# Kernel optimization log

Measured on AMD Instinct MI355X. Metric: run time of the kernel, lower is better.

Reference implementation:

```python
import jax, jax.numpy as jnp
import numpy as np

N = 100000
E = 1600000
IN_DIM = 128
EDGE_DIM = 32
H = 4
C = 32  # out_vertex_dim per head; concat output = H*C = 128


def setup_inputs() -> dict:
    key = jax.random.key(0)
    ks = jax.random.split(key, 12)
    point_attr = jax.random.normal(ks[0], (N, IN_DIM), dtype=jnp.float32)
    edge_index = jax.random.randint(ks[1], (2, E), 0, N, dtype=jnp.int64)
    edge_attr = jax.random.normal(ks[2], (E, EDGE_DIM), dtype=jnp.float32)
    # GATConv params (lin shared for src/dst when in_channels is int; bias separate)
    g = lambda k, shp, fan: jax.random.normal(k, shp, dtype=jnp.float32) * np.float32(1.0 / np.sqrt(fan))
    W = g(ks[3], (IN_DIM, H * C), IN_DIM)          # lin weight (no bias in PyG GATConv lin)
    att_src = g(ks[4], (H, C), C)
    att_dst = g(ks[5], (H, C), C)
    W_edge = g(ks[6], (EDGE_DIM, H * C), EDGE_DIM)  # lin_edge (bias=False)
    att_edge = g(ks[7], (H, C), C)
    bias = jnp.zeros((H * C,), dtype=jnp.float32)
    ln_gamma = jnp.ones((H * C,), dtype=jnp.float32)
    ln_beta = jnp.zeros((H * C,), dtype=jnp.float32)
    return {"point_attr": point_attr, "edge_index": edge_index, "edge_attr": edge_attr,
            "W": W, "att_src": att_src, "att_dst": att_dst, "W_edge": W_edge,
            "att_edge": att_edge, "bias": bias, "ln_gamma": ln_gamma, "ln_beta": ln_beta}


def reference(point_attr, edge_index, edge_attr, W, att_src, att_dst, W_edge, att_edge, bias, ln_gamma, ln_beta):
    n = point_attr.shape[0]
    x = (point_attr @ W).reshape(n, H, C)                      # [N,H,C]
    a_src = jnp.sum(x * att_src[None], axis=-1)                # [N,H]
    a_dst = jnp.sum(x * att_dst[None], axis=-1)                # [N,H]
    src, dst = edge_index[0], edge_index[1]
    e = (edge_attr @ W_edge).reshape(-1, H, C)                 # [E,H,C]
    a_edge = jnp.sum(e * att_edge[None], axis=-1)              # [E,H]
    alpha = a_src[src] + a_dst[dst] + a_edge                   # [E,H]
    alpha = jax.nn.leaky_relu(alpha, 0.2)                      # GATConv negative_slope
    amax = jax.ops.segment_max(alpha, dst, num_segments=n)
    expa = jnp.exp(alpha - amax[dst])
    asum = jax.ops.segment_sum(expa, dst, num_segments=n)
    attw = expa / (asum[dst] + 1e-16)                          # segment softmax over dst
    msg = x[src] * attw[:, :, None]                            # [E,H,C] gather+scale
    out = jax.ops.segment_sum(msg, dst, num_segments=n).reshape(n, H * C) + bias
    # LayerNorm(H*C)
    mu = jnp.mean(out, axis=-1, keepdims=True)
    var = jnp.mean((out - mu) ** 2, axis=-1, keepdims=True)
    out = (out - mu) / jnp.sqrt(var + 1e-5) * ln_gamma + ln_beta
    return jax.nn.leaky_relu(out, 0.01)                        # nn.LeakyReLU default slope
```

## Files before the change

kernel.cpp:

```cpp
#include <hip/hip_runtime.h>
#include <hip/hip_bf16.h>

#define IN_DIM 128
#define HC 128
#define NH 4
#define CH 32
#define EDGE_DIM 32
#define CAP 48

typedef short s8v __attribute__((ext_vector_type(8)));
typedef float f4v __attribute__((ext_vector_type(4)));

__device__ __forceinline__ unsigned pack_bf16(float a, float b) {
    unsigned ua = __float_as_uint(a), ub = __float_as_uint(b);
    ua += 0x7fffu + ((ua >> 16) & 1u);
    ub += 0x7fffu + ((ub >> 16) & 1u);
    return (ua >> 16) | (ub & 0xffff0000u);
}
__device__ __forceinline__ unsigned short bf16_1(float a) {
    unsigned ua = __float_as_uint(a);
    ua += 0x7fffu + ((ua >> 16) & 1u);
    return (unsigned short)(ua >> 16);
}

__global__ __launch_bounds__(256) void k_vp(
    const float* __restrict__ W_edge, const float* __restrict__ att_edge,
    float* __restrict__ v_edge, const float* __restrict__ W,
    unsigned short* __restrict__ Wt)
{
    int b = blockIdx.x, t = threadIdx.x;
    if (b == 64) {
        if (t < 128) {
            int h = t >> 5, k = t & 31;
            float s = 0.f;
            #pragma unroll
            for (int c = 0; c < CH; ++c)
                s += W_edge[k * HC + h * CH + c] * att_edge[h * CH + c];
            v_edge[h * EDGE_DIM + k] = s;
        }
    } else {
        int id = b * 256 + t;
        int n = id >> 7, k = id & 127;
        Wt[n * 128 + k] = bf16_1(W[k * 128 + n]);
    }
}

__global__ __launch_bounds__(256) void k_phase1(
    const float* __restrict__ edge_attr, const int* __restrict__ ei,
    const float* __restrict__ v_edge, int* __restrict__ cnt,
    int4* __restrict__ slots,
    const float* __restrict__ A, const unsigned short* __restrict__ Wt,
    unsigned short* __restrict__ xb16, int N, int E, int nbEdge)
{
    __shared__ unsigned Al[64 * 64];
    __shared__ float vl[HC];

    int t = threadIdx.x;

    if (blockIdx.x < nbEdge) {
        if (t < HC) vl[t] = v_edge[t];
        __syncthreads();
        int e = blockIdx.x * 256 + t;
        if (e >= E) return;
        const float4* ea4 = (const float4*)edge_attr + (size_t)e * 8;
        float ae[4] = {0.f, 0.f, 0.f, 0.f};
        #pragma unroll
        for (int j = 0; j < 8; ++j) {
            float4 v = ea4[j];
            #pragma unroll
            for (int h = 0; h < 4; ++h) {
                const float* vh = &vl[h * 32 + j * 4];
                ae[h] += v.x * vh[0] + v.y * vh[1] + v.z * vh[2] + v.w * vh[3];
            }
        }
        int src = ei[e], dst = ei[E + e];
        int pos = atomicAdd(&cnt[dst], 1);
        if (pos < CAP) {
            int4 pk;
            pk.x = src;
            pk.y = (int)pack_bf16(ae[0], ae[1]);
            pk.z = (int)pack_bf16(ae[2], ae[3]);
            pk.w = 0;
            slots[(size_t)dst * CAP + pos] = pk;
        }
    } else {
        int node0 = (blockIdx.x - nbEdge) * 64;
        const float4* A4 = (const float4*)A;
        #pragma unroll
        for (int it = 0; it < 8; ++it) {
            int id = it * 256 + t;
            int row = id >> 5, c = id & 31;
            float4 v = {0.f, 0.f, 0.f, 0.f};
            if (node0 + row < N) v = A4[(size_t)(node0 + row) * 32 + c];
            unsigned u0 = pack_bf16(v.x, v.y);
            unsigned u1 = pack_bf16(v.z, v.w);
            int k2 = 2 * c;
            int slot = k2 >> 2;
            int idx = ((slot ^ (row & 15)) << 2) | (k2 & 3);
            Al[row * 64 + idx]     = u0;
            Al[row * 64 + idx + 1] = u1;
        }
        __syncthreads();

        int l = t & 63;
        int w = t >> 6;
        int lrow = l & 15;
        int lk   = l >> 4;

        s8v afr[4];
        #pragma unroll
        for (int kb = 0; kb < 4; ++kb) {
            int slot = kb * 4 + lk;
            const unsigned* p = &Al[(w * 16 + lrow) * 64 + ((slot ^ lrow) << 2)];
            afr[kb] = *(const s8v*)p;
        }

        #pragma unroll
        for (int ct = 0; ct < 8; ++ct) {
            int col = ct * 16 + lrow;
            f4v acc = {0.f, 0.f, 0.f, 0.f};
            #pragma unroll
            for (int kb = 0; kb < 4; ++kb) {
                s8v bfr = *(const s8v*)&Wt[col * 128 + kb * 32 + lk * 8];
                acc = __builtin_amdgcn_mfma_f32_16x16x32_bf16(afr[kb], bfr, acc, 0, 0, 0);
            }
            #pragma unroll
            for (int r = 0; r < 4; ++r) {
                int node = node0 + w * 16 + lk * 4 + r;
                if (node < N) xb16[(size_t)node * 128 + col] = bf16_1(acc[r]);
            }
        }
    }
}

__global__ __launch_bounds__(256) void k_att(
    const unsigned* __restrict__ xb, const float* __restrict__ att_src,
    const float* __restrict__ att_dst, float* __restrict__ a_src,
    float* __restrict__ a_dst, int N)
{
    int t = threadIdx.x;
    int node = blockIdx.x * 16 + (t >> 4);
    int lane = t & 15;
    if (node >= N) return;
    const uint4* x4 = (const uint4*)xb;
    uint4 xv = x4[(size_t)node * 16 + lane];
    int c = lane * 8;
    float xs[8];
    xs[0] = __uint_as_float(xv.x << 16); xs[1] = __uint_as_float(xv.x & 0xffff0000u);
    xs[2] = __uint_as_float(xv.y << 16); xs[3] = __uint_as_float(xv.y & 0xffff0000u);
    xs[4] = __uint_as_float(xv.z << 16); xs[5] = __uint_as_float(xv.z & 0xffff0000u);
    xs[6] = __uint_as_float(xv.w << 16); xs[7] = __uint_as_float(xv.w & 0xffff0000u);
    float ps = 0.f, pd = 0.f;
    #pragma unroll
    for (int i = 0; i < 8; ++i) {
        ps += xs[i] * att_src[c + i];
        pd += xs[i] * att_dst[c + i];
    }
    ps += __shfl_xor(ps, 1); ps += __shfl_xor(ps, 2);
    pd += __shfl_xor(pd, 1); pd += __shfl_xor(pd, 2);
    if ((lane & 3) == 0) {
        a_src[node * 4 + (lane >> 2)] = ps;
        a_dst[node * 4 + (lane >> 2)] = pd;
    }
}

__global__ __launch_bounds__(256) void k_agg(
    const int* __restrict__ cnt, const int4* __restrict__ slots,
    const float* __restrict__ a_src, const float* __restrict__ a_dst,
    const unsigned* __restrict__ xb, const float* __restrict__ bias,
    const float* __restrict__ gamma, const float* __restrict__ beta,
    float* __restrict__ out, int N)
{
    int t = threadIdx.x;
    int node = blockIdx.x * 16 + (t >> 4);
    int lane = t & 15;
    if (node >= N) return;
    int st = node * CAP;
    int deg = cnt[node]; if (deg > CAP) deg = CAP;
    int en = st + deg;
    int hsel = lane >> 2;
    float adst = a_dst[node * 4 + hsel];
    const uint4* x4 = (const uint4*)xb;
    float acc[8] = {0.f, 0.f, 0.f, 0.f, 0.f, 0.f, 0.f, 0.f};
    float denom = 0.f;

    int s_c[4]; float ae_c[4], as_c[4];

    if (st < en) {
        #pragma unroll
        for (int j = 0; j < 4; ++j) {
            bool v = (st + j) < en;
            int a = v ? (st + j) : st;
            int4 pk = slots[a];
            s_c[j] = pk.x;
            unsigned w = (hsel & 2) ? (unsigned)pk.z : (unsigned)pk.y;
            float e = __uint_as_float((hsel & 1) ? (w & 0xffff0000u) : (w << 16));
            ae_c[j] = v ? e : -1e30f;
        }
        #pragma unroll
        for (int j = 0; j < 4; ++j) as_c[j] = a_src[s_c[j] * 4 + hsel];

        for (int p = st; p < en; p += 4) {
            int pn = p + 4;
            int s_n[4]; float ae_n[4], as_n[4];
            #pragma unroll
            for (int j = 0; j < 4; ++j) {
                bool v = (pn + j) < en;
                int a = v ? (pn + j) : st;
                int4 pk = slots[a];
                s_n[j] = pk.x;
                unsigned w = (hsel & 2) ? (unsigned)pk.z : (unsigned)pk.y;
                float e = __uint_as_float((hsel & 1) ? (w & 0xffff0000u) : (w << 16));
                ae_n[j] = v ? e : -1e30f;
            }
            #pragma unroll
            for (int j = 0; j < 4; ++j) as_n[j] = a_src[s_n[j] * 4 + hsel];

            #pragma unroll
            for (int j = 0; j < 4; ++j) {
                float al = as_c[j] + adst + ae_c[j];
                al = (al < 0.f) ? 0.2f * al : al;
                float ex = __expf(al);
                denom += ex;
                uint4 xv = x4[(size_t)s_c[j] * 16 + lane];
                acc[0] += ex * __uint_as_float(xv.x << 16);
                acc[1] += ex * __uint_as_float(xv.x & 0xffff0000u);
                acc[2] += ex * __uint_as_float(xv.y << 16);
                acc[3] += ex * __uint_as_float(xv.y & 0xffff0000u);
                acc[4] += ex * __uint_as_float(xv.z << 16);
                acc[5] += ex * __uint_as_float(xv.z & 0xffff0000u);
                acc[6] += ex * __uint_as_float(xv.w << 16);
                acc[7] += ex * __uint_as_float(xv.w & 0xffff0000u);
            }
            #pragma unroll
            for (int j = 0; j < 4; ++j) {
                s_c[j] = s_n[j]; ae_c[j] = ae_n[j]; as_c[j] = as_n[j];
            }
        }
    }
    float inv = 1.f / (denom + 1e-16f);
    int c = lane * 8;
    float4 b0 = *(const float4*)&bias[c];
    float4 b1 = *(const float4*)&bias[c + 4];
    float o[8];
    o[0] = acc[0] * inv + b0.x; o[1] = acc[1] * inv + b0.y;
    o[2] = acc[2] * inv + b0.z; o[3] = acc[3] * inv + b0.w;
    o[4] = acc[4] * inv + b1.x; o[5] = acc[5] * inv + b1.y;
    o[6] = acc[6] * inv + b1.z; o[7] = acc[7] * inv + b1.w;

    float s = 0.f;
    #pragma unroll
    for (int i = 0; i < 8; ++i) s += o[i];
    #pragma unroll
    for (int m = 1; m < 16; m <<= 1) s += __shfl_xor(s, m, 16);
    float mu = s * (1.0f / 128.0f);
    float q = 0.f;
    #pragma unroll
    for (int i = 0; i < 8; ++i) { o[i] -= mu; q += o[i] * o[i]; }
    #pragma unroll
    for (int m = 1; m < 16; m <<= 1) q += __shfl_xor(q, m, 16);
    float rstd = rsqrtf(q * (1.0f / 128.0f) + 1e-5f);
    float4 g0 = *(const float4*)&gamma[c];
    float4 g1 = *(const float4*)&gamma[c + 4];
    float4 e0 = *(const float4*)&beta[c];
    float4 e1 = *(const float4*)&beta[c + 4];
    float y[8];
    y[0] = o[0] * rstd * g0.x + e0.x; y[1] = o[1] * rstd * g0.y + e0.y;
    y[2] = o[2] * rstd * g0.z + e0.z; y[3] = o[3] * rstd * g0.w + e0.w;
    y[4] = o[4] * rstd * g1.x + e1.x; y[5] = o[5] * rstd * g1.y + e1.y;
    y[6] = o[6] * rstd * g1.z + e1.z; y[7] = o[7] * rstd * g1.w + e1.w;
    #pragma unroll
    for (int i = 0; i < 8; ++i) y[i] = (y[i] < 0.f) ? 0.01f * y[i] : y[i];
    float4 r0 = {y[0], y[1], y[2], y[3]};
    float4 r1 = {y[4], y[5], y[6], y[7]};
    float4* op = (float4*)out + (size_t)node * 32 + lane * 2;
    op[0] = r0;
    op[1] = r1;
}

extern "C" void kernel_launch(void* const* d_in, const int* in_sizes, int n_in,
                              void* d_out, int out_size, void* d_ws, size_t ws_size,
                              hipStream_t stream) {
    const float* point_attr = (const float*)d_in[0];
    const int*   edge_index = (const int*)d_in[1];
    const float* edge_attr  = (const float*)d_in[2];
    const float* W          = (const float*)d_in[3];
    const float* att_src    = (const float*)d_in[4];
    const float* att_dst    = (const float*)d_in[5];
    const float* W_edge     = (const float*)d_in[6];
    const float* att_edge   = (const float*)d_in[7];
    const float* bias       = (const float*)d_in[8];
    const float* ln_gamma   = (const float*)d_in[9];
    const float* ln_beta    = (const float*)d_in[10];

    int N = in_sizes[0] / IN_DIM;
    int E = in_sizes[2] / EDGE_DIM;
    float* out = (float*)d_out;

    char* ws = (char*)d_ws;
    size_t off = 0;
    auto alloc = [&](size_t bytes) {
        void* p = ws + off;
        off += (bytes + 255) & ~(size_t)255;
        return p;
    };
    unsigned* xb     = (unsigned*)alloc((size_t)N * 128 * 2);
    float* a_src     = (float*)alloc((size_t)N * 4 * 4);
    float* a_dst     = (float*)alloc((size_t)N * 4 * 4);
    int*   cnt       = (int*)alloc((size_t)N * 4);
    float* v_edge    = (float*)alloc(128 * 4);
    unsigned short* Wt = (unsigned short*)alloc(128 * 128 * 2);
    int4*  slots     = (int4*)alloc((size_t)N * CAP * 16);

    hipMemsetAsync(cnt, 0, (size_t)N * 4, stream);

    int nbEdge = (E + 255) / 256;
    int nbGemm = (N + 63) / 64;
    int nbAtt  = (N + 15) / 16;

    k_vp<<<65, 256, 0, stream>>>(W_edge, att_edge, v_edge, W, Wt);
    k_phase1<<<nbEdge + nbGemm, 256, 0, stream>>>(
        edge_attr, edge_index, v_edge, cnt, slots,
        point_attr, Wt, (unsigned short*)xb, N, E, nbEdge);
    k_att<<<nbAtt, 256, 0, stream>>>(xb, att_src, att_dst, a_src, a_dst, N);
    k_agg<<<nbAtt, 256, 0, stream>>>(cnt, slots, a_src, a_dst, xb,
                                     bias, ln_gamma, ln_beta, out, N);
}
```

Measured before the change: 247.6 us.

## Fuse attention-score dot products into GEMM epilogue and stage edge_attr through LDS

Removes the separate k_att kernel. a_src and a_dst are now computed from the fp32 MFMA accumulators in the projection GEMM's epilogue and reduced with cross-lane shuffles, which saves a launch and a full re-read of the bf16 x buffer. In the edge path, each block now loads its edge_attr tile with coalesced float4 reads into XOR-swizzled shared memory, replacing per-thread strided 128-byte row reads. In exchange, shared memory per block rises to about 33 KB and register pressure in the GEMM path goes up. The attention scores are also computed from unrounded fp32 values instead of bf16 x.

```diff
diff --git a/kernel.cpp b/kernel.cpp
--- a/kernel.cpp
+++ b/kernel.cpp
@@ -50,28 +50,46 @@
     const float* __restrict__ v_edge, int* __restrict__ cnt,
     int4* __restrict__ slots,
     const float* __restrict__ A, const unsigned short* __restrict__ Wt,
-    unsigned short* __restrict__ xb16, int N, int E, int nbEdge)
+    unsigned short* __restrict__ xb16,
+    const float* __restrict__ att_src, const float* __restrict__ att_dst,
+    float* __restrict__ a_src, float* __restrict__ a_dst,
+    int N, int E, int nbEdge)
 {
-    __shared__ unsigned Al[64 * 64];
-    __shared__ float vl[HC];
-
+    __shared__ __align__(16) char smem_[32768 + 512];
     int t = threadIdx.x;
 
     if (blockIdx.x < nbEdge) {
+        float* se = (float*)smem_;
+        float* vl = (float*)(smem_ + 32768);
+
+        const float4* eab4 = (const float4*)edge_attr + (size_t)blockIdx.x * 2048;
+        int rem = E - blockIdx.x * 256;
+        int nf4 = (rem >= 256) ? 2048 : ((rem > 0) ? rem * 8 : 0);
+        #pragma unroll
+        for (int it = 0; it < 8; ++it) {
+            int idx = it * 256 + t;
+            float4 f = {0.f, 0.f, 0.f, 0.f};
+            if (idx < nf4) f = eab4[idx];
+            int edge = idx >> 3, p4 = idx & 7, sw = edge & 31;
+            float* bp = &se[edge * 32];
+            bp[(p4 * 4 + 0) ^ sw] = f.x;
+            bp[(p4 * 4 + 1) ^ sw] = f.y;
+            bp[(p4 * 4 + 2) ^ sw] = f.z;
+            bp[(p4 * 4 + 3) ^ sw] = f.w;
+        }
         if (t < HC) vl[t] = v_edge[t];
         __syncthreads();
+
         int e = blockIdx.x * 256 + t;
         if (e >= E) return;
-        const float4* ea4 = (const float4*)edge_attr + (size_t)e * 8;
+        int sw = t & 31;
+        const float* bp = &se[t * 32];
         float ae[4] = {0.f, 0.f, 0.f, 0.f};
         #pragma unroll
-        for (int j = 0; j < 8; ++j) {
-            float4 v = ea4[j];
-            #pragma unroll
-            for (int h = 0; h < 4; ++h) {
-                const float* vh = &vl[h * 32 + j * 4];
-                ae[h] += v.x * vh[0] + v.y * vh[1] + v.z * vh[2] + v.w * vh[3];
-            }
+        for (int i = 0; i < 32; ++i) {
+            float x = bp[i ^ sw];
+            #pragma unroll
+            for (int h = 0; h < 4; ++h) ae[h] += x * vl[h * 32 + i];
         }
         int src = ei[e], dst = ei[E + e];
         int pos = atomicAdd(&cnt[dst], 1);
@@ -84,6 +102,7 @@
             slots[(size_t)dst * CAP + pos] = pk;
         }
     } else {
+        unsigned* Al = (unsigned*)smem_;
         int node0 = (blockIdx.x - nbEdge) * 64;
         const float4* A4 = (const float4*)A;
         #pragma unroll
@@ -115,6 +134,12 @@
             afr[kb] = *(const s8v*)p;
         }
 
+        float ps[4][4], pd[4][4];
+        #pragma unroll
+        for (int r = 0; r < 4; ++r)
+            #pragma unroll
+            for (int h = 0; h < 4; ++h) { ps[r][h] = 0.f; pd[r][h] = 0.f; }
+
         #pragma unroll
         for (int ct = 0; ct < 8; ++ct) {
             int col = ct * 16 + lrow;
@@ -124,43 +149,43 @@
                 s8v bfr = *(const s8v*)&Wt[col * 128 + kb * 32 + lk * 8];
                 acc = __builtin_amdgcn_mfma_f32_16x16x32_bf16(afr[kb], bfr, acc, 0, 0, 0);
             }
+            float av = att_src[col], dv = att_dst[col];
+            #pragma unroll
+            for (int r = 0; r < 4; ++r) {
+                ps[r][ct >> 1] += acc[r] * av;
+                pd[r][ct >> 1] += acc[r] * dv;
+            }
             #pragma unroll
             for (int r = 0; r < 4; ++r) {
                 int node = node0 + w * 16 + lk * 4 + r;
                 if (node < N) xb16[(size_t)node * 128 + col] = bf16_1(acc[r]);
             }
         }
-    }
-}
-
-__global__ __launch_bounds__(256) void k_att(
-    const unsigned* __restrict__ xb, const float* __restrict__ att_src,
-    const float* __restrict__ att_dst, float* __restrict__ a_src,
-    float* __restrict__ a_dst, int N)
-{
-    int t = threadIdx.x;
-    int node = blockIdx.x * 16 + (t >> 4);
-    int lane = t & 15;
-    if (node >= N) return;
-    const uint4* x4 = (const uint4*)xb;
-    uint4 xv = x4[(size_t)node * 16 + lane];
-    int c = lane * 8;
-    float xs[8];
-    xs[0] = __uint_as_float(xv.x << 16); xs[1] = __uint_as_float(xv.x & 0xffff0000u);
-    xs[2] = __uint_as_float(xv.y << 16); xs[3] = __uint_as_float(xv.y & 0xffff0000u);
-    xs[4] = __uint_as_float(xv.z << 16); xs[5] = __uint_as_float(xv.z & 0xffff0000u);
-    xs[6] = __uint_as_float(xv.w << 16); xs[7] = __uint_as_float(xv.w & 0xffff0000u);
-    float ps = 0.f, pd = 0.f;
-    #pragma unroll
-    for (int i = 0; i < 8; ++i) {
-        ps += xs[i] * att_src[c + i];
-        pd += xs[i] * att_dst[c + i];
-    }
-    ps += __shfl_xor(ps, 1); ps += __shfl_xor(ps, 2);
-    pd += __shfl_xor(pd, 1); pd += __shfl_xor(pd, 2);
-    if ((lane & 3) == 0) {
-        a_src[node * 4 + (lane >> 2)] = ps;
-        a_dst[node * 4 + (lane >> 2)] = pd;
+
+        #pragma unroll
+        for (int r = 0; r < 4; ++r)
+            #pragma unroll
+            for (int h = 0; h < 4; ++h) {
+                float vs = ps[r][h], vd = pd[r][h];
+                #pragma unroll
+                for (int m = 1; m <= 8; m <<= 1) {
+                    vs += __shfl_xor(vs, m);
+                    vd += __shfl_xor(vd, m);
+                }
+                ps[r][h] = vs; pd[r][h] = vd;
+            }
+        if (lrow == 0) {
+            #pragma unroll
+            for (int r = 0; r < 4; ++r) {
+                int node = node0 + w * 16 + lk * 4 + r;
+                if (node < N) {
+                    float4 vs = {ps[r][0], ps[r][1], ps[r][2], ps[r][3]};
+                    float4 vd = {pd[r][0], pd[r][1], pd[r][2], pd[r][3]};
+                    *(float4*)&a_src[node * 4] = vs;
+                    *(float4*)&a_dst[node * 4] = vd;
+                }
+            }
+        }
     }
 }
 
@@ -321,8 +346,8 @@
     k_vp<<<65, 256, 0, stream>>>(W_edge, att_edge, v_edge, W, Wt);
     k_phase1<<<nbEdge + nbGemm, 256, 0, stream>>>(
         edge_attr, edge_index, v_edge, cnt, slots,
-        point_attr, Wt, (unsigned short*)xb, N, E, nbEdge);
-    k_att<<<nbAtt, 256, 0, stream>>>(xb, att_src, att_dst, a_src, a_dst, N);
+        point_attr, Wt, (unsigned short*)xb, att_src, att_dst,
+        a_src, a_dst, N, E, nbEdge);
     k_agg<<<nbAtt, 256, 0, stream>>>(cnt, slots, a_src, a_dst, xb,
                                      bias, ln_gamma, ln_beta, out, N);
 }
```

New measurement: 250.1 us. About the same (+1.0%).
